# Optimization experiments

Measured on AMD Instinct MI355X. Metric: run time of the kernel, lower is better.

## Reference

```python
import jax, jax.numpy as jnp
import numpy as np

B, T, E, D = 64, 512, 1024, 1024  # batch, enc timesteps, enc hidden, dec hidden


def setup_inputs() -> dict:
    key = jax.random.key(0)
    ks = jax.random.split(key, 9)
    s = lambda fan_in: 1.0 / np.sqrt(fan_in)
    return {
        "hidden": jax.random.normal(ks[0], (B, D), jnp.float32),
        "decoder_out": jax.random.normal(ks[1], (B, D), jnp.float32),
        "encoder_states": jax.random.normal(ks[2], (T, B, E), jnp.float32),
        # attn: Linear(D+E -> 2E)
        "Wa": jax.random.uniform(ks[3], (2 * E, D + E), jnp.float32, -s(D + E), s(D + E)),
        "ba": jax.random.uniform(ks[4], (2 * E,), jnp.float32, -s(D + E), s(D + E)),
        # attn2: Linear(2E -> 1)
        "w2": jax.random.uniform(ks[5], (1, 2 * E), jnp.float32, -s(2 * E), s(2 * E)),
        "b2": jax.random.uniform(ks[6], (1,), jnp.float32, -s(2 * E), s(2 * E)),
        # attn_combine: Linear(D+E -> D)
        "Wc": jax.random.uniform(ks[7], (D, D + E), jnp.float32, -s(D + E), s(D + E)),
        "bc": jax.random.uniform(ks[8], (D,), jnp.float32, -s(D + E), s(D + E)),
    }


def reference(hidden, decoder_out, encoder_states, Wa, ba, w2, b2, Wc, bc):
    d = hidden.shape[1]
    # attn(cat(hidden, enc_t)) = hidden @ Wa[:, :D].T + enc_t @ Wa[:, D:].T + ba
    h_proj = hidden @ Wa[:, :d].T + ba                      # [B, 2E]
    e_proj = jnp.einsum('tbe,fe->tbf', encoder_states, Wa[:, d:])  # [T, B, 2E]
    act = jnp.tanh(h_proj[None, :, :] + e_proj)             # [T, B, 2E]
    scores = jnp.einsum('tbf,f->bt', act, w2[0]) + b2[0]    # [B, T]
    weights = jax.nn.softmax(scores, axis=-1)               # softmax over timesteps
    # weighted sum of encoder states: [B, E]
    applied = jnp.einsum('bt,tbe->be', weights, encoder_states)
    combined = jnp.concatenate([decoder_out, applied], axis=1)  # [B, D+E]
    out = jnp.tanh(combined @ Wc.T + bc)                    # [B, D]
    return out, applied
```

## Files before the change

### kernel.cpp

```cpp
#include <hip/hip_runtime.h>
#include <hip/hip_bf16.h>

#define BB 64
#define TT 512
#define EE 1024
#define DD 1024
#define BK 64

typedef __attribute__((ext_vector_type(8))) short s16x8;
typedef __attribute__((ext_vector_type(4))) float f32x4;

#define AS1 __attribute__((address_space(1)))
#define AS3 __attribute__((address_space(3)))

__device__ __forceinline__ float bf2f(unsigned short u) {
    unsigned int x = ((unsigned int)u) << 16;
    return __builtin_bit_cast(float, x);
}
__device__ __forceinline__ unsigned short f2bf(float f) {
    unsigned int u = __builtin_bit_cast(unsigned int, f);
    u += 0x7FFF + ((u >> 16) & 1);
    return (unsigned short)(u >> 16);
}
__device__ __forceinline__ float tanh_fast(float x) {
    x = fminf(fmaxf(x, -15.f), 15.f);
    float e = __expf(2.f * x);
    return (e - 1.f) / (e + 1.f);
}

__device__ __forceinline__ int tile_slot(int row, int g) {
    return (row >> 4) * 128 + (g >> 2) * 64 + (g & 3) * 16 + (row & 15);
}

__global__ __launch_bounds__(256) void conv_encS_kernel(
    const float* __restrict__ enc, unsigned short* __restrict__ encS)
{
    __shared__ short tileL[1024 * 8];
    const int tm  = blockIdx.x;
    const int tk  = blockIdx.y;
    const int tid = threadIdx.x;

#pragma unroll
    for (int it = 0; it < 4; ++it) {
        int cidx = it * 256 + tid;
        int row  = cidx >> 3;
        int g    = cidx & 7;
        const float* src = enc + (size_t)(tm * 128 + row) * 1024 + tk * 64 + g * 8;
        float4 v0 = ((const float4*)src)[0];
        float4 v1 = ((const float4*)src)[1];
        short c[8];
        c[0] = (short)f2bf(v0.x); c[1] = (short)f2bf(v0.y);
        c[2] = (short)f2bf(v0.z); c[3] = (short)f2bf(v0.w);
        c[4] = (short)f2bf(v1.x); c[5] = (short)f2bf(v1.y);
        c[6] = (short)f2bf(v1.z); c[7] = (short)f2bf(v1.w);
        *(s16x8*)&tileL[tile_slot(row, g) * 8] = *(s16x8*)c;
    }
    __syncthreads();
    unsigned short* dst = encS + ((size_t)tm * 16 + tk) * 8192;
#pragma unroll
    for (int it = 0; it < 4; ++it) {
        int s = it * 256 + tid;
        *(s16x8*)&dst[s * 8] = *(const s16x8*)&tileL[s * 8];
    }
}

__global__ __launch_bounds__(256) void conv_waS_kernel(
    const float* __restrict__ Wa, unsigned short* __restrict__ WaS)
{
    __shared__ short tileL[1024 * 8];
    const int tn  = blockIdx.x;
    const int tk  = blockIdx.y;
    const int tid = threadIdx.x;

#pragma unroll
    for (int it = 0; it < 4; ++it) {
        int cidx = it * 256 + tid;
        int row  = cidx >> 3;
        int g    = cidx & 7;
        const float* src = Wa + (size_t)(tn * 128 + row) * 2048 + 1024 + tk * 64 + g * 8;
        float4 v0 = ((const float4*)src)[0];
        float4 v1 = ((const float4*)src)[1];
        short c[8];
        c[0] = (short)f2bf(v0.x); c[1] = (short)f2bf(v0.y);
        c[2] = (short)f2bf(v0.z); c[3] = (short)f2bf(v0.w);
        c[4] = (short)f2bf(v1.x); c[5] = (short)f2bf(v1.y);
        c[6] = (short)f2bf(v1.z); c[7] = (short)f2bf(v1.w);
        *(s16x8*)&tileL[tile_slot(row, g) * 8] = *(s16x8*)c;
    }
    __syncthreads();
    unsigned short* dst = WaS + ((size_t)tn * 16 + tk) * 8192;
#pragma unroll
    for (int it = 0; it < 4; ++it) {
        int s = it * 256 + tid;
        *(s16x8*)&dst[s * 8] = *(const s16x8*)&tileL[s * 8];
    }
}

__global__ __launch_bounds__(256) void hproj_kernel(
    const float* __restrict__ hidden,
    const float* __restrict__ Wa,
    const float* __restrict__ ba,
    float* __restrict__ hp)
{
    __shared__ float sW[8 * 1024];
    const int tid  = threadIdx.x;
    const int lane = tid & 63;
    const int wave = tid >> 6;
    const int f0   = blockIdx.x * 8;

#pragma unroll
    for (int i = 0; i < 8; ++i) {
        int idx = i * 256 + tid;
        int fi  = idx >> 8;
        int c4  = idx & 255;
        ((float4*)sW)[idx] = *(const float4*)(Wa + (size_t)(f0 + fi) * 2048 + c4 * 4);
    }
    __syncthreads();

    for (int bi = 0; bi < 16; ++bi) {
        int b = wave * 16 + bi;
        float h[16];
#pragma unroll
        for (int j = 0; j < 16; ++j) h[j] = hidden[b * 1024 + lane + 64 * j];
#pragma unroll
        for (int fi = 0; fi < 8; ++fi) {
            float s = 0.f;
#pragma unroll
            for (int j = 0; j < 16; ++j) s += h[j] * sW[fi * 1024 + lane + 64 * j];
#pragma unroll
            for (int m = 32; m; m >>= 1) s += __shfl_xor(s, m);
            if (lane == 0) hp[(f0 + fi) * 64 + b] = s + ba[f0 + fi];
        }
    }
}

__global__ __launch_bounds__(1024) void gemm_scores(
    const unsigned short* __restrict__ encS,
    const unsigned short* __restrict__ WaS,
    const float* __restrict__ hp,
    const float* __restrict__ w2,
    float* __restrict__ scores)
{
    __shared__ short sA[2][2][8192];
    __shared__ short sB[2][2][8192];
    __shared__ float rowAcc[256];

    const int tid  = threadIdx.x;
    const int bid  = blockIdx.x;
    const int w    = (bid & 7) * 128 + (bid >> 3);
    const int bm   = w >> 3;
    const int bn   = w & 7;
    const int lane = tid & 63;
    const int wave = tid >> 6;
    const int wm   = wave >> 2;
    const int wn   = wave & 3;
    const int c    = lane & 15;
    const int quad = lane >> 4;
    const int mt   = wm >> 1;
    const int mrow0 = (wm & 1) * 4;
    const int nt   = wn >> 1;
    const int nrow0 = (wn & 1) * 4;

    f32x4 acc[4][4];
#pragma unroll
    for (int m = 0; m < 4; ++m)
#pragma unroll
        for (int n = 0; n < 4; ++n)
#pragma unroll
            for (int r = 0; r < 4; ++r) acc[m][n][r] = 0.f;

    const unsigned short* aT = encS + ((size_t)(bm * 2) * 16) * 8192;
    const unsigned short* bT = WaS  + ((size_t)(bn * 2) * 16) * 8192;

    auto STAGE_ALL = [&](int kt, int nb) {
#pragma unroll
        for (int t = 0; t < 2; ++t) {
            const unsigned short* sa = aT + ((size_t)(t * 16 + kt)) * 8192;
            __builtin_amdgcn_global_load_lds(
                (const AS1 void*)(sa + tid * 8),
                (AS3 void*)&sA[nb][t][tid * 8], 16, 0, 0);
            const unsigned short* sb = bT + ((size_t)(t * 16 + kt)) * 8192;
            __builtin_amdgcn_global_load_lds(
                (const AS1 void*)(sb + tid * 8),
                (AS3 void*)&sB[nb][t][tid * 8], 16, 0, 0);
        }
    };

    STAGE_ALL(0, 0);

    for (int kt = 0; kt < 16; ++kt) {
        const int cur = kt & 1;
        asm volatile("s_waitcnt vmcnt(0)" ::: "memory");
        __builtin_amdgcn_s_barrier();
        __builtin_amdgcn_sched_barrier(0);
        if (kt < 15) STAGE_ALL(kt + 1, cur ^ 1);

#pragma unroll
        for (int kk = 0; kk < 2; ++kk) {
            s16x8 aF[4], bF[4];
#pragma unroll
            for (int m = 0; m < 4; ++m)
                aF[m] = *(const s16x8*)
                    &sA[cur][mt][((mrow0 + m) * 128 + kk * 64 + lane) * 8];
#pragma unroll
            for (int n = 0; n < 4; ++n)
                bF[n] = *(const s16x8*)
                    &sB[cur][nt][((nrow0 + n) * 128 + kk * 64 + lane) * 8];

            __builtin_amdgcn_s_setprio(1);
#pragma unroll
            for (int m = 0; m < 4; ++m)
#pragma unroll
                for (int n = 0; n < 4; ++n)
                    acc[m][n] = __builtin_amdgcn_mfma_f32_16x16x32_bf16(
                        aF[m], bF[n], acc[m][n], 0, 0, 0);
            __builtin_amdgcn_s_setprio(0);
        }
        __builtin_amdgcn_sched_barrier(0);
        __builtin_amdgcn_s_barrier();
    }

    if (tid < 256) rowAcc[tid] = 0.f;
    __syncthreads();

    float w2v[4];
#pragma unroll
    for (int n = 0; n < 4; ++n) w2v[n] = w2[bn * 256 + wn * 64 + n * 16 + c];

#pragma unroll
    for (int m = 0; m < 4; ++m) {
        int lrow0 = wm * 64 + m * 16 + quad * 4;
        int b0    = lrow0 & 63;
        f32x4 hp4[4];
#pragma unroll
        for (int n = 0; n < 4; ++n)
            hp4[n] = *(const f32x4*)&hp[(bn * 256 + wn * 64 + n * 16 + c) * 64 + b0];
#pragma unroll
        for (int r = 0; r < 4; ++r) {
            float s = 0.f;
#pragma unroll
            for (int n = 0; n < 4; ++n)
                s += tanh_fast(acc[m][n][r] + hp4[n][r]) * w2v[n];
            s += __shfl_xor(s, 1);
            s += __shfl_xor(s, 2);
            s += __shfl_xor(s, 4);
            s += __shfl_xor(s, 8);
            if (c == 0) atomicAdd(&rowAcc[lrow0 + r], s);
        }
    }
    __syncthreads();
    if (tid < 256) {
        int b = tid & 63;
        int t = bm * 4 + (tid >> 6);
        atomicAdd(&scores[b * TT + t], rowAcc[tid]);
    }
}

__global__ __launch_bounds__(256) void softmax_kernel(float* __restrict__ scores)
{
    __shared__ float wmax[4];
    __shared__ float wsum[4];
    const int b   = blockIdx.x;
    const int tid = threadIdx.x;
    float* row = scores + b * TT;

    float v0 = row[tid], v1 = row[tid + 256];
    float m = fmaxf(v0, v1);
#pragma unroll
    for (int s = 32; s; s >>= 1) m = fmaxf(m, __shfl_xor(m, s));
    if ((tid & 63) == 0) wmax[tid >> 6] = m;
    __syncthreads();
    m = fmaxf(fmaxf(wmax[0], wmax[1]), fmaxf(wmax[2], wmax[3]));

    float e0 = __expf(v0 - m), e1 = __expf(v1 - m);
    float s = e0 + e1;
#pragma unroll
    for (int t = 32; t; t >>= 1) s += __shfl_xor(s, t);
    if ((tid & 63) == 0) wsum[tid >> 6] = s;
    __syncthreads();
    float inv = 1.f / (wsum[0] + wsum[1] + wsum[2] + wsum[3]);
    row[tid]       = e0 * inv;
    row[tid + 256] = e1 * inv;
}

__global__ __launch_bounds__(256) void applied_part_kernel(
    const float* __restrict__ enc,
    const float* __restrict__ w,
    float* __restrict__ part)
{
    __shared__ float red[128 * 8];
    const int tc  = blockIdx.x;
    const int b   = blockIdx.y;
    const int tid = threadIdx.x;
    const int eo  = tid & 127;
    const int th  = tid >> 7;
    const int e0  = eo * 8;

    float a[8];
#pragma unroll
    for (int j = 0; j < 8; ++j) a[j] = 0.f;

    for (int it = 0; it < 16; ++it) {
        int t = tc * 32 + th * 16 + it;
        float wt = w[b * TT + t];
        const float* src = enc + ((size_t)(t * BB + b)) * EE + e0;
        float4 v0 = ((const float4*)src)[0];
        float4 v1 = ((const float4*)src)[1];
        a[0] += wt * v0.x; a[1] += wt * v0.y; a[2] += wt * v0.z; a[3] += wt * v0.w;
        a[4] += wt * v1.x; a[5] += wt * v1.y; a[6] += wt * v1.z; a[7] += wt * v1.w;
    }
    if (th == 1) {
#pragma unroll
        for (int j = 0; j < 8; ++j) red[eo * 8 + j] = a[j];
    }
    __syncthreads();
    if (th == 0) {
        float* dst = part + ((size_t)tc * 64 + b) * 1024 + e0;
#pragma unroll
        for (int j = 0; j < 8; ++j) dst[j] = a[j] + red[eo * 8 + j];
    }
}

__global__ __launch_bounds__(256) void applied_reduce_kernel(
    const float* __restrict__ part, float* __restrict__ out_applied)
{
    int idx = blockIdx.x * 256 + threadIdx.x;
    float s = 0.f;
#pragma unroll
    for (int tc = 0; tc < 16; ++tc) s += part[tc * 65536 + idx];
    out_applied[idx] = s;
}

__global__ __launch_bounds__(256) void combine_kernel(
    const float* __restrict__ dec,
    const float* applied,
    const float* __restrict__ Wc,
    const float* __restrict__ bc,
    float* out0)
{
    const int gw   = blockIdx.x * 4 + (threadIdx.x >> 6);
    const int lane = threadIdx.x & 63;
    const int d0   = (gw >> 3) * 8;
    const int b0   = (gw & 7) * 8;

    float acc[8][8];
#pragma unroll
    for (int dd = 0; dd < 8; ++dd)
#pragma unroll
        for (int bb = 0; bb < 8; ++bb) acc[dd][bb] = 0.f;

#pragma unroll
    for (int j = 0; j < 8; ++j) {
        float4 wv[8];
#pragma unroll
        for (int dd = 0; dd < 8; ++dd)
            wv[dd] = ((const float4*)(Wc + (size_t)(d0 + dd) * 2048))[j * 64 + lane];
        float4 cv[8];
        if (j < 4) {
#pragma unroll
            for (int bb = 0; bb < 8; ++bb)
                cv[bb] = ((const float4*)(dec + (size_t)(b0 + bb) * 1024))[j * 64 + lane];
        } else {
#pragma unroll
            for (int bb = 0; bb < 8; ++bb)
                cv[bb] = ((const float4*)(applied + (size_t)(b0 + bb) * 1024))[(j - 4) * 64 + lane];
        }
#pragma unroll
        for (int dd = 0; dd < 8; ++dd)
#pragma unroll
            for (int bb = 0; bb < 8; ++bb)
                acc[dd][bb] += wv[dd].x * cv[bb].x + wv[dd].y * cv[bb].y
                             + wv[dd].z * cv[bb].z + wv[dd].w * cv[bb].w;
    }

#pragma unroll
    for (int dd = 0; dd < 8; ++dd) {
#pragma unroll
        for (int bb = 0; bb < 8; ++bb) {
            float s = acc[dd][bb];
#pragma unroll
            for (int m = 32; m; m >>= 1) s += __shfl_xor(s, m);
            if (lane == 0)
                out0[(size_t)(b0 + bb) * DD + d0 + dd] = tanh_fast(s + bc[d0 + dd]);
        }
    }
}

extern "C" void kernel_launch(void* const* d_in, const int* in_sizes, int n_in,
                              void* d_out, int out_size, void* d_ws, size_t ws_size,
                              hipStream_t stream) {
    const float* hidden = (const float*)d_in[0];
    const float* dec    = (const float*)d_in[1];
    const float* enc    = (const float*)d_in[2];
    const float* Wa     = (const float*)d_in[3];
    const float* ba     = (const float*)d_in[4];
    const float* w2     = (const float*)d_in[5];
    const float* Wc     = (const float*)d_in[7];
    const float* bc     = (const float*)d_in[8];
    float* out = (float*)d_out;

    unsigned short* encS = (unsigned short*)d_ws;
    unsigned short* WaS  = encS + (size_t)33554432;
    float* hp     = (float*)(WaS + (size_t)2097152);
    float* scores = hp + 131072;
    float* part   = scores + 32768;

    hipMemsetAsync(scores, 0, BB * TT * sizeof(float), stream);
    dim3 gc(256, 16);
    conv_encS_kernel<<<gc, 256, 0, stream>>>(enc, encS);
    dim3 gw(16, 16);
    conv_waS_kernel<<<gw, 256, 0, stream>>>(Wa, WaS);
    hproj_kernel<<<256, 256, 0, stream>>>(hidden, Wa, ba, hp);
    gemm_scores<<<1024, 1024, 0, stream>>>(encS, WaS, hp, w2, scores);
    softmax_kernel<<<BB, 256, 0, stream>>>(scores);
    dim3 g3(16, 64);
    applied_part_kernel<<<g3, 256, 0, stream>>>(enc, scores, part);
    applied_reduce_kernel<<<256, 256, 0, stream>>>(part, out + BB * DD);
    combine_kernel<<<256, 256, 0, stream>>>(dec, out + BB * DD, Wc, bc, out);
}
```

Before: 511.8 us.

## Fuse prep kernels, replace score atomics with partials, fold softmax into applied kernel

Merges the Wa bf16 conversion and hidden projection into one launch, splitting the work by block index. The score GEMM now writes per-column-block partial scores instead of doing atomicAdds, which removes the memset. The softmax kernel is dropped: each applied_part block sums the eight partials and recomputes the softmax for its batch row in shared memory. This cuts three launches and the atomics, at the cost of every applied block redundantly reading 8x512 partials and recomputing the softmax.

```diff
diff --git a/kernel.cpp b/kernel.cpp
--- a/kernel.cpp
+++ b/kernel.cpp
@@ -5,7 +5,6 @@
 #define TT 512
 #define EE 1024
 #define DD 1024
-#define BK 64
 
 typedef __attribute__((ext_vector_type(8))) short s16x8;
 typedef __attribute__((ext_vector_type(4))) float f32x4;
@@ -13,10 +12,6 @@
 #define AS1 __attribute__((address_space(1)))
 #define AS3 __attribute__((address_space(3)))
 
-__device__ __forceinline__ float bf2f(unsigned short u) {
-    unsigned int x = ((unsigned int)u) << 16;
-    return __builtin_bit_cast(float, x);
-}
 __device__ __forceinline__ unsigned short f2bf(float f) {
     unsigned int u = __builtin_bit_cast(unsigned int, f);
     u += 0x7FFF + ((u >> 16) & 1);
@@ -64,72 +59,69 @@
     }
 }
 
-__global__ __launch_bounds__(256) void conv_waS_kernel(
-    const float* __restrict__ Wa, unsigned short* __restrict__ WaS)
-{
-    __shared__ short tileL[1024 * 8];
-    const int tn  = blockIdx.x;
-    const int tk  = blockIdx.y;
+__global__ __launch_bounds__(256) void prep_kernel(
+    const float* __restrict__ Wa,
+    const float* __restrict__ hidden,
+    const float* __restrict__ ba,
+    unsigned short* __restrict__ WaS,
+    float* __restrict__ hp)
+{
+    __shared__ float smem[8 * 1024];
+    const int bid = blockIdx.x;
     const int tid = threadIdx.x;
 
-#pragma unroll
-    for (int it = 0; it < 4; ++it) {
-        int cidx = it * 256 + tid;
-        int row  = cidx >> 3;
-        int g    = cidx & 7;
-        const float* src = Wa + (size_t)(tn * 128 + row) * 2048 + 1024 + tk * 64 + g * 8;
-        float4 v0 = ((const float4*)src)[0];
-        float4 v1 = ((const float4*)src)[1];
-        short c[8];
-        c[0] = (short)f2bf(v0.x); c[1] = (short)f2bf(v0.y);
-        c[2] = (short)f2bf(v0.z); c[3] = (short)f2bf(v0.w);
-        c[4] = (short)f2bf(v1.x); c[5] = (short)f2bf(v1.y);
-        c[6] = (short)f2bf(v1.z); c[7] = (short)f2bf(v1.w);
-        *(s16x8*)&tileL[tile_slot(row, g) * 8] = *(s16x8*)c;
-    }
-    __syncthreads();
-    unsigned short* dst = WaS + ((size_t)tn * 16 + tk) * 8192;
-#pragma unroll
-    for (int it = 0; it < 4; ++it) {
-        int s = it * 256 + tid;
-        *(s16x8*)&dst[s * 8] = *(const s16x8*)&tileL[s * 8];
-    }
-}
-
-__global__ __launch_bounds__(256) void hproj_kernel(
-    const float* __restrict__ hidden,
-    const float* __restrict__ Wa,
-    const float* __restrict__ ba,
-    float* __restrict__ hp)
-{
-    __shared__ float sW[8 * 1024];
-    const int tid  = threadIdx.x;
-    const int lane = tid & 63;
-    const int wave = tid >> 6;
-    const int f0   = blockIdx.x * 8;
-
-#pragma unroll
-    for (int i = 0; i < 8; ++i) {
-        int idx = i * 256 + tid;
-        int fi  = idx >> 8;
-        int c4  = idx & 255;
-        ((float4*)sW)[idx] = *(const float4*)(Wa + (size_t)(f0 + fi) * 2048 + c4 * 4);
-    }
-    __syncthreads();
-
-    for (int bi = 0; bi < 16; ++bi) {
-        int b = wave * 16 + bi;
-        float h[16];
-#pragma unroll
-        for (int j = 0; j < 16; ++j) h[j] = hidden[b * 1024 + lane + 64 * j];
-#pragma unroll
-        for (int fi = 0; fi < 8; ++fi) {
-            float s = 0.f;
-#pragma unroll
-            for (int j = 0; j < 16; ++j) s += h[j] * sW[fi * 1024 + lane + 64 * j];
-#pragma unroll
-            for (int m = 32; m; m >>= 1) s += __shfl_xor(s, m);
-            if (lane == 0) hp[(f0 + fi) * 64 + b] = s + ba[f0 + fi];
+    if (bid < 256) {
+        short* tileL = (short*)smem;
+        const int tn = bid & 15;
+        const int tk = bid >> 4;
+#pragma unroll
+        for (int it = 0; it < 4; ++it) {
+            int cidx = it * 256 + tid;
+            int row  = cidx >> 3;
+            int g    = cidx & 7;
+            const float* src = Wa + (size_t)(tn * 128 + row) * 2048 + 1024 + tk * 64 + g * 8;
+            float4 v0 = ((const float4*)src)[0];
+            float4 v1 = ((const float4*)src)[1];
+            short c[8];
+            c[0] = (short)f2bf(v0.x); c[1] = (short)f2bf(v0.y);
+            c[2] = (short)f2bf(v0.z); c[3] = (short)f2bf(v0.w);
+            c[4] = (short)f2bf(v1.x); c[5] = (short)f2bf(v1.y);
+            c[6] = (short)f2bf(v1.z); c[7] = (short)f2bf(v1.w);
+            *(s16x8*)&tileL[tile_slot(row, g) * 8] = *(s16x8*)c;
+        }
+        __syncthreads();
+        unsigned short* dst = WaS + ((size_t)tn * 16 + tk) * 8192;
+#pragma unroll
+        for (int it = 0; it < 4; ++it) {
+            int s = it * 256 + tid;
+            *(s16x8*)&dst[s * 8] = *(const s16x8*)&tileL[s * 8];
+        }
+    } else {
+        const int lane = tid & 63;
+        const int wave = tid >> 6;
+        const int f0   = (bid - 256) * 8;
+#pragma unroll
+        for (int i = 0; i < 8; ++i) {
+            int idx = i * 256 + tid;
+            int fi  = idx >> 8;
+            int c4  = idx & 255;
+            ((float4*)smem)[idx] = *(const float4*)(Wa + (size_t)(f0 + fi) * 2048 + c4 * 4);
+        }
+        __syncthreads();
+        for (int bi = 0; bi < 16; ++bi) {
+            int b = wave * 16 + bi;
+            float h[16];
+#pragma unroll
+            for (int j = 0; j < 16; ++j) h[j] = hidden[b * 1024 + lane + 64 * j];
+#pragma unroll
+            for (int fi = 0; fi < 8; ++fi) {
+                float s = 0.f;
+#pragma unroll
+                for (int j = 0; j < 16; ++j) s += h[j] * smem[fi * 1024 + lane + 64 * j];
+#pragma unroll
+                for (int m = 32; m; m >>= 1) s += __shfl_xor(s, m);
+                if (lane == 0) hp[(f0 + fi) * 64 + b] = s + ba[f0 + fi];
+            }
         }
     }
 }
@@ -139,7 +131,7 @@
     const unsigned short* __restrict__ WaS,
     const float* __restrict__ hp,
     const float* __restrict__ w2,
-    float* __restrict__ scores)
+    float* __restrict__ scoresP)
 {
     __shared__ short sA[2][2][8192];
     __shared__ short sB[2][2][8192];
@@ -252,43 +244,18 @@
     if (tid < 256) {
         int b = tid & 63;
         int t = bm * 4 + (tid >> 6);
-        atomicAdd(&scores[b * TT + t], rowAcc[tid]);
-    }
-}
-
-__global__ __launch_bounds__(256) void softmax_kernel(float* __restrict__ scores)
-{
-    __shared__ float wmax[4];
-    __shared__ float wsum[4];
-    const int b   = blockIdx.x;
-    const int tid = threadIdx.x;
-    float* row = scores + b * TT;
-
-    float v0 = row[tid], v1 = row[tid + 256];
-    float m = fmaxf(v0, v1);
-#pragma unroll
-    for (int s = 32; s; s >>= 1) m = fmaxf(m, __shfl_xor(m, s));
-    if ((tid & 63) == 0) wmax[tid >> 6] = m;
-    __syncthreads();
-    m = fmaxf(fmaxf(wmax[0], wmax[1]), fmaxf(wmax[2], wmax[3]));
-
-    float e0 = __expf(v0 - m), e1 = __expf(v1 - m);
-    float s = e0 + e1;
-#pragma unroll
-    for (int t = 32; t; t >>= 1) s += __shfl_xor(s, t);
-    if ((tid & 63) == 0) wsum[tid >> 6] = s;
-    __syncthreads();
-    float inv = 1.f / (wsum[0] + wsum[1] + wsum[2] + wsum[3]);
-    row[tid]       = e0 * inv;
-    row[tid + 256] = e1 * inv;
+        scoresP[((size_t)bn * 64 + b) * 512 + t] = rowAcc[tid];
+    }
 }
 
 __global__ __launch_bounds__(256) void applied_part_kernel(
     const float* __restrict__ enc,
-    const float* __restrict__ w,
+    const float* __restrict__ scoresP,
     float* __restrict__ part)
 {
     __shared__ float red[128 * 8];
+    __shared__ float sw[512];
+    __shared__ float red4[4];
     const int tc  = blockIdx.x;
     const int b   = blockIdx.y;
     const int tid = threadIdx.x;
@@ -296,13 +263,40 @@
     const int th  = tid >> 7;
     const int e0  = eo * 8;
 
+    {
+        const int t0 = tid * 2;
+        float s0 = 0.f, s1 = 0.f;
+#pragma unroll
+        for (int bn = 0; bn < 8; ++bn) {
+            const float* sp = scoresP + ((size_t)bn * 64 + b) * 512;
+            s0 += sp[t0]; s1 += sp[t0 + 1];
+        }
+        float m = fmaxf(s0, s1);
+#pragma unroll
+        for (int o = 32; o; o >>= 1) m = fmaxf(m, __shfl_xor(m, o));
+        if ((tid & 63) == 0) red4[tid >> 6] = m;
+        __syncthreads();
+        m = fmaxf(fmaxf(red4[0], red4[1]), fmaxf(red4[2], red4[3]));
+        __syncthreads();
+        float e0v = __expf(s0 - m), e1v = __expf(s1 - m);
+        float ss = e0v + e1v;
+#pragma unroll
+        for (int o = 32; o; o >>= 1) ss += __shfl_xor(ss, o);
+        if ((tid & 63) == 0) red4[tid >> 6] = ss;
+        __syncthreads();
+        float inv = 1.f / (red4[0] + red4[1] + red4[2] + red4[3]);
+        sw[t0]     = e0v * inv;
+        sw[t0 + 1] = e1v * inv;
+        __syncthreads();
+    }
+
     float a[8];
 #pragma unroll
     for (int j = 0; j < 8; ++j) a[j] = 0.f;
 
     for (int it = 0; it < 16; ++it) {
         int t = tc * 32 + th * 16 + it;
-        float wt = w[b * TT + t];
+        float wt = sw[t];
         const float* src = enc + ((size_t)(t * BB + b)) * EE + e0;
         float4 v0 = ((const float4*)src)[0];
         float4 v1 = ((const float4*)src)[1];
@@ -401,20 +395,16 @@
 
     unsigned short* encS = (unsigned short*)d_ws;
     unsigned short* WaS  = encS + (size_t)33554432;
-    float* hp     = (float*)(WaS + (size_t)2097152);
-    float* scores = hp + 131072;
-    float* part   = scores + 32768;
-
-    hipMemsetAsync(scores, 0, BB * TT * sizeof(float), stream);
+    float* hp      = (float*)(WaS + (size_t)2097152);
+    float* scoresP = hp + 131072;
+    float* part    = scoresP + 262144;
+
     dim3 gc(256, 16);
     conv_encS_kernel<<<gc, 256, 0, stream>>>(enc, encS);
-    dim3 gw(16, 16);
-    conv_waS_kernel<<<gw, 256, 0, stream>>>(Wa, WaS);
-    hproj_kernel<<<256, 256, 0, stream>>>(hidden, Wa, ba, hp);
-    gemm_scores<<<1024, 1024, 0, stream>>>(encS, WaS, hp, w2, scores);
-    softmax_kernel<<<BB, 256, 0, stream>>>(scores);
+    prep_kernel<<<512, 256, 0, stream>>>(Wa, hidden, ba, WaS, hp);
+    gemm_scores<<<1024, 1024, 0, stream>>>(encS, WaS, hp, w2, scoresP);
     dim3 g3(16, 64);
-    applied_part_kernel<<<g3, 256, 0, stream>>>(enc, scores, part);
+    applied_part_kernel<<<g3, 256, 0, stream>>>(enc, scoresP, part);
     applied_reduce_kernel<<<256, 256, 0, stream>>>(part, out + BB * DD);
     combine_kernel<<<256, 256, 0, stream>>>(dec, out + BB * DD, Wc, bc, out);
 }
```

New measurement: 515.2 us. Within noise of the previous version (+0.7%).
